# Performance work log

Measured on AMD Instinct MI355X. Metric: run time of the kernel, lower is better.

## Reference

```python
import jax, jax.numpy as jnp
import numpy as np

LATENT_DIM = 512
BATCH = 1024


def setup_inputs() -> dict:
    key = jax.random.key(0)
    k1, k2 = jax.random.split(key)
    ctrl_latent = jax.random.normal(k1, (BATCH, LATENT_DIM), dtype=jnp.float32)
    weights = jax.random.normal(k2, (LATENT_DIM, LATENT_DIM), dtype=jnp.float32)
    bias = jnp.zeros((LATENT_DIM,), dtype=jnp.float32)
    return {"ctrl_latent": ctrl_latent, "weights": weights, "bias": bias}


def reference(ctrl_latent, weights, bias):
    # Math (eval mode, dropout = identity):
    #   pred[b, i] = sum_j x[b, i] * x[b, j] * W[i, j] + bias[i]
    # Fused form avoiding the (batch, d, d) intermediate:
    #   pred = x * (x @ W.T) + bias
    wx = jnp.einsum('bj,ij->bi', ctrl_latent, weights)  # (B, d)
    return ctrl_latent * wx + bias
```

## Files before the change

### kernel.cpp

```cpp
#include <hip/hip_runtime.h>
#include <stdint.h>


#define LATENT 512
#define BATCH  1024
#define BM 64
#define BN 32
#define BK 64
#define LDK (BK + 8)

typedef short bf16x8 __attribute__((ext_vector_type(8)));
typedef float f32x4  __attribute__((ext_vector_type(4)));

__device__ __forceinline__ short f2bf(float f) {
    uint32_t u = __builtin_bit_cast(uint32_t, f);
    u += 0x7FFFu + ((u >> 16) & 1u);
    return (short)(u >> 16);
}

__global__ __launch_bounds__(128) void filnp_kernel(
    const float* __restrict__ X, const float* __restrict__ W,
    const float* __restrict__ bias, float* __restrict__ out)
{
    __shared__ short As[BM][LDK];
    __shared__ short Bs[BN][LDK];

    const int tid  = threadIdx.x;
    const int lane = tid & 63;
    const int wv   = tid >> 6;
    const int n0   = blockIdx.x * BN;
    const int m0   = blockIdx.y * BM;

    const int qrow = lane >> 4;
    const int lrow = lane & 15;

    f32x4 acc[2][2] = {};

    const int ar = tid >> 1;
    const int ac = (tid & 1) * 32;
    const int br = tid >> 2;
    const int bc = (tid & 3) * 16;

    for (int kt = 0; kt < LATENT / BK; ++kt) {
        const int k0 = kt * BK;

        {
            const float* src = X + (size_t)(m0 + ar) * LATENT + k0 + ac;
            float av[32];
            #pragma unroll
            for (int i = 0; i < 8; ++i)
                ((f32x4*)av)[i] = ((const f32x4*)src)[i];
            short bv[32];
            #pragma unroll
            for (int i = 0; i < 32; ++i) bv[i] = f2bf(av[i]);
            #pragma unroll
            for (int i = 0; i < 4; ++i)
                *(bf16x8*)&As[ar][ac + i * 8] = ((bf16x8*)bv)[i];
        }
        {
            const float* src = W + (size_t)(n0 + br) * LATENT + k0 + bc;
            float av[16];
            #pragma unroll
            for (int i = 0; i < 4; ++i)
                ((f32x4*)av)[i] = ((const f32x4*)src)[i];
            short bv[16];
            #pragma unroll
            for (int i = 0; i < 16; ++i) bv[i] = f2bf(av[i]);
            #pragma unroll
            for (int i = 0; i < 2; ++i)
                *(bf16x8*)&Bs[br][bc + i * 8] = ((bf16x8*)bv)[i];
        }
        __syncthreads();

        #pragma unroll
        for (int ks = 0; ks < BK / 32; ++ks) {
            const int kc = ks * 32 + qrow * 8;
            bf16x8 a0 = *(const bf16x8*)&As[wv * 32 +      lrow][kc];
            bf16x8 a1 = *(const bf16x8*)&As[wv * 32 + 16 + lrow][kc];
            bf16x8 b0 = *(const bf16x8*)&Bs[     lrow][kc];
            bf16x8 b1 = *(const bf16x8*)&Bs[16 + lrow][kc];
            acc[0][0] = __builtin_amdgcn_mfma_f32_16x16x32_bf16(a0, b0, acc[0][0], 0, 0, 0);
            acc[0][1] = __builtin_amdgcn_mfma_f32_16x16x32_bf16(a0, b1, acc[0][1], 0, 0, 0);
            acc[1][0] = __builtin_amdgcn_mfma_f32_16x16x32_bf16(a1, b0, acc[1][0], 0, 0, 0);
            acc[1][1] = __builtin_amdgcn_mfma_f32_16x16x32_bf16(a1, b1, acc[1][1], 0, 0, 0);
        }
        __syncthreads();
    }

    #pragma unroll
    for (int mi = 0; mi < 2; ++mi) {
        #pragma unroll
        for (int ni = 0; ni < 2; ++ni) {
            #pragma unroll
            for (int r = 0; r < 4; ++r) {
                const int m = m0 + wv * 32 + mi * 16 + qrow * 4 + r;
                const int n = n0 + ni * 16 + lrow;
                const float wx = acc[mi][ni][r];
                out[(size_t)m * LATENT + n] = X[(size_t)m * LATENT + n] * wx + bias[n];
            }
        }
    }
}

extern "C" void kernel_launch(void* const* d_in, const int* in_sizes, int n_in,
                              void* d_out, int out_size, void* d_ws, size_t ws_size,
                              hipStream_t stream) {
    const float* X    = (const float*)d_in[0];
    const float* W    = (const float*)d_in[1];
    const float* bias = (const float*)d_in[2];
    float* out        = (float*)d_out;

    dim3 grid(LATENT / BN, BATCH / BM);
    filnp_kernel<<<grid, 128, 0, stream>>>(X, W, bias, out);
}
```

Before: 69.33 us.

## Pre-convert inputs to bf16 in a separate pass and read MFMA operands directly

Adds a conversion kernel that writes X and W as bf16 into workspace, then runs a GEMM kernel whose waves load MFMA fragments straight from global bf16 memory with no LDS staging or barriers. Each wave computes one 16x16 output tile over the full K dimension. This removes the repeated fp32 loads and conversions that the old tiled kernel did for every block, and removes the synchronisation. In exchange it adds a second kernel launch and a round trip through global memory for the converted data, and operand reuse now relies on the cache rather than shared memory.

```diff
diff --git a/kernel.cpp b/kernel.cpp
--- a/kernel.cpp
+++ b/kernel.cpp
@@ -4,10 +4,8 @@
 
 #define LATENT 512
 #define BATCH  1024
-#define BM 64
-#define BN 32
-#define BK 64
-#define LDK (BK + 8)
+#define XN (BATCH * LATENT)
+#define WN (LATENT * LATENT)
 
 typedef short bf16x8 __attribute__((ext_vector_type(8)));
 typedef float f32x4  __attribute__((ext_vector_type(4)));
@@ -18,87 +16,54 @@
     return (short)(u >> 16);
 }
 
-__global__ __launch_bounds__(128) void filnp_kernel(
+__global__ __launch_bounds__(256) void convert_kernel(
     const float* __restrict__ X, const float* __restrict__ W,
-    const float* __restrict__ bias, float* __restrict__ out)
+    short* __restrict__ Xb, short* __restrict__ Wb)
 {
-    __shared__ short As[BM][LDK];
-    __shared__ short Bs[BN][LDK];
+    const int g = (blockIdx.x * 256 + threadIdx.x) * 8;
+    const float* src;
+    short* dst;
+    if (g < XN) { src = X + g;        dst = Xb + g; }
+    else        { src = W + (g - XN); dst = Wb + (g - XN); }
+    f32x4 v0 = ((const f32x4*)src)[0];
+    f32x4 v1 = ((const f32x4*)src)[1];
+    short s[8];
+    #pragma unroll
+    for (int i = 0; i < 4; ++i) s[i]     = f2bf(v0[i]);
+    #pragma unroll
+    for (int i = 0; i < 4; ++i) s[4 + i] = f2bf(v1[i]);
+    *(bf16x8*)dst = *(bf16x8*)s;
+}
 
+__global__ __launch_bounds__(256) void gemm_kernel(
+    const short* __restrict__ Xb, const short* __restrict__ Wb,
+    const float* __restrict__ X, const float* __restrict__ bias,
+    float* __restrict__ out)
+{
     const int tid  = threadIdx.x;
     const int lane = tid & 63;
     const int wv   = tid >> 6;
-    const int n0   = blockIdx.x * BN;
-    const int m0   = blockIdx.y * BM;
+    const int m0   = blockIdx.y * 32 + (wv >> 1) * 16;
+    const int n0   = blockIdx.x * 32 + (wv & 1) * 16;
+    const int lrow = lane & 15;
+    const int q    = lane >> 4;
 
-    const int qrow = lane >> 4;
-    const int lrow = lane & 15;
+    const short* ap = Xb + (size_t)(m0 + lrow) * LATENT + q * 8;
+    const short* bp = Wb + (size_t)(n0 + lrow) * LATENT + q * 8;
 
-    f32x4 acc[2][2] = {};
-
-    const int ar = tid >> 1;
-    const int ac = (tid & 1) * 32;
-    const int br = tid >> 2;
-    const int bc = (tid & 3) * 16;
-
-    for (int kt = 0; kt < LATENT / BK; ++kt) {
-        const int k0 = kt * BK;
-
-        {
-            const float* src = X + (size_t)(m0 + ar) * LATENT + k0 + ac;
-            float av[32];
-            #pragma unroll
-            for (int i = 0; i < 8; ++i)
-                ((f32x4*)av)[i] = ((const f32x4*)src)[i];
-            short bv[32];
-            #pragma unroll
-            for (int i = 0; i < 32; ++i) bv[i] = f2bf(av[i]);
-            #pragma unroll
-            for (int i = 0; i < 4; ++i)
-                *(bf16x8*)&As[ar][ac + i * 8] = ((bf16x8*)bv)[i];
-        }
-        {
-            const float* src = W + (size_t)(n0 + br) * LATENT + k0 + bc;
-            float av[16];
-            #pragma unroll
-            for (int i = 0; i < 4; ++i)
-                ((f32x4*)av)[i] = ((const f32x4*)src)[i];
-            short bv[16];
-            #pragma unroll
-            for (int i = 0; i < 16; ++i) bv[i] = f2bf(av[i]);
-            #pragma unroll
-            for (int i = 0; i < 2; ++i)
-                *(bf16x8*)&Bs[br][bc + i * 8] = ((bf16x8*)bv)[i];
-        }
-        __syncthreads();
-
-        #pragma unroll
-        for (int ks = 0; ks < BK / 32; ++ks) {
-            const int kc = ks * 32 + qrow * 8;
-            bf16x8 a0 = *(const bf16x8*)&As[wv * 32 +      lrow][kc];
-            bf16x8 a1 = *(const bf16x8*)&As[wv * 32 + 16 + lrow][kc];
-            bf16x8 b0 = *(const bf16x8*)&Bs[     lrow][kc];
-            bf16x8 b1 = *(const bf16x8*)&Bs[16 + lrow][kc];
-            acc[0][0] = __builtin_amdgcn_mfma_f32_16x16x32_bf16(a0, b0, acc[0][0], 0, 0, 0);
-            acc[0][1] = __builtin_amdgcn_mfma_f32_16x16x32_bf16(a0, b1, acc[0][1], 0, 0, 0);
-            acc[1][0] = __builtin_amdgcn_mfma_f32_16x16x32_bf16(a1, b0, acc[1][0], 0, 0, 0);
-            acc[1][1] = __builtin_amdgcn_mfma_f32_16x16x32_bf16(a1, b1, acc[1][1], 0, 0, 0);
-        }
-        __syncthreads();
+    f32x4 acc = {};
+    #pragma unroll
+    for (int ks = 0; ks < 16; ++ks) {
+        bf16x8 a = *(const bf16x8*)(ap + ks * 32);
+        bf16x8 b = *(const bf16x8*)(bp + ks * 32);
+        acc = __builtin_amdgcn_mfma_f32_16x16x32_bf16(a, b, acc, 0, 0, 0);
     }
 
     #pragma unroll
-    for (int mi = 0; mi < 2; ++mi) {
-        #pragma unroll
-        for (int ni = 0; ni < 2; ++ni) {
-            #pragma unroll
-            for (int r = 0; r < 4; ++r) {
-                const int m = m0 + wv * 32 + mi * 16 + qrow * 4 + r;
-                const int n = n0 + ni * 16 + lrow;
-                const float wx = acc[mi][ni][r];
-                out[(size_t)m * LATENT + n] = X[(size_t)m * LATENT + n] * wx + bias[n];
-            }
-        }
+    for (int r = 0; r < 4; ++r) {
+        const int m = m0 + q * 4 + r;
+        const int n = n0 + lrow;
+        out[(size_t)m * LATENT + n] = X[(size_t)m * LATENT + n] * acc[r] + bias[n];
     }
 }
 
@@ -110,6 +75,9 @@
     const float* bias = (const float*)d_in[2];
     float* out        = (float*)d_out;
 
-    dim3 grid(LATENT / BN, BATCH / BM);
-    filnp_kernel<<<grid, 128, 0, stream>>>(X, W, bias, out);
+    short* Xb = (short*)d_ws;
+    short* Wb = (short*)d_ws + XN;
+
+    convert_kernel<<<(XN + WN) / 8 / 256, 256, 0, stream>>>(X, W, Xb, Wb);
+    gemm_kernel<<<dim3(LATENT / 32, BATCH / 32), 256, 0, stream>>>(Xb, Wb, X, bias, out);
 }
```

New measurement: 67.49 us. 1.03x faster.
